# Kernel tuning notes

Hardware: AMD Instinct MI355X
Metric: run time of the kernel (lower is better)

## Reference

```python
import jax, jax.numpy as jnp
import numpy as np

N_QUBITS = 12
N_LAYERS = 6
N_CLASSES = 10
BATCH = 4096


def _rot_matrix(phi, theta, omega):
    # PennyLane Rot(phi, theta, omega) = RZ(omega) @ RY(theta) @ RZ(phi)
    ct = jnp.cos(theta / 2).astype(jnp.complex64)
    st = jnp.sin(theta / 2).astype(jnp.complex64)
    ep = jnp.exp(-0.5j * (phi + omega)).astype(jnp.complex64)  # e^{-i(phi+omega)/2}
    em = jnp.exp(-0.5j * (phi - omega)).astype(jnp.complex64)  # e^{-i(phi-omega)/2}
    row0 = jnp.stack([ep * ct, -jnp.conj(em) * st])
    row1 = jnp.stack([em * st, jnp.conj(ep) * ct])
    return jnp.stack([row0, row1])  # [2, 2] complex64


def _apply_1q(state, U, q):
    # state: [B] + [2]*n ; apply 2x2 gate U on qubit axis q
    s = jnp.moveaxis(state, q + 1, -1)
    s = jnp.einsum('...i,ji->...j', s, U)
    return jnp.moveaxis(s, -1, q + 1)


def _apply_cnot(state, c, t):
    # flip target axis where control bit == 1
    s = jnp.moveaxis(state, (c + 1, t + 1), (1, 2))
    s = jnp.concatenate([s[:, :1], jnp.flip(s[:, 1:2], axis=2)], axis=1)
    return jnp.moveaxis(s, (1, 2), (c + 1, t + 1))


def _pauliz_signs(n):
    idx = np.arange(2 ** n)
    bits = (idx[None, :] >> (n - 1 - np.arange(n))[:, None]) & 1  # [n, 2^n]
    return jnp.asarray(1.0 - 2.0 * bits, dtype=jnp.float32)


def _quantum_forward(x, q_params):
    B, n = x.shape
    # rotation encoding: RY(x_q)|0> = [cos(x/2), sin(x/2)] -> product state
    c = jnp.cos(x / 2)
    s = jnp.sin(x / 2)
    state = jnp.ones((B, 1), dtype=jnp.complex64)
    for q in range(n):
        amp = jnp.stack([c[:, q], s[:, q]], axis=-1).astype(jnp.complex64)  # [B, 2]
        state = (state[:, :, None] * amp[:, None, :]).reshape(B, -1)
    state = state.reshape((B,) + (2,) * n)
    # StronglyEntanglingLayers: per-layer Rot on every wire, then CNOT ring with range r
    for l in range(N_LAYERS):
        for q in range(n):
            U = _rot_matrix(q_params[l, q, 0], q_params[l, q, 1], q_params[l, q, 2])
            state = _apply_1q(state, U, q)
        r = (l % (n - 1)) + 1
        for q in range(n):
            state = _apply_cnot(state, q, (q + r) % n)
    probs = (jnp.abs(state) ** 2).reshape(B, -1).astype(jnp.float32)  # [B, 2^n]
    signs = _pauliz_signs(n)  # [n, 2^n]
    return probs @ signs.T  # PauliZ expvals, [B, n]


def setup_inputs() -> dict:
    key = jax.random.key(0)
    k1, k2, k3, k4 = jax.random.split(key, 4)
    x = jax.random.normal(k1, (BATCH, N_QUBITS), dtype=jnp.float32)
    q_params = 0.01 * jax.random.normal(k2, (N_LAYERS, N_QUBITS, 3), dtype=jnp.float32)
    lim = 1.0 / np.sqrt(N_QUBITS)
    fc_w = jax.random.uniform(k3, (N_CLASSES, N_QUBITS), jnp.float32, -lim, lim)
    fc_b = jax.random.uniform(k4, (N_CLASSES,), jnp.float32, -lim, lim)
    return {"x": x, "q_params": q_params, "fc_w": fc_w, "fc_b": fc_b}


def reference(x, q_params, fc_w, fc_b):
    expvals = _quantum_forward(x, q_params)  # [B, n_qubits]
    return expvals @ fc_w.T + fc_b  # logits [B, n_classes]
```

## Files before the change

kernel.cpp:

```cpp
#include <hip/hip_runtime.h>
#include <hip/hip_fp16.h>

#define NQ 12
#define NL 6
#define NC 10
#define DIM 4096
#define TPB 256
#define NPASS 18

typedef _Float16 half8_t __attribute__((ext_vector_type(8)));
typedef __fp16 fp16x2 __attribute__((ext_vector_type(2)));
typedef float f32x4 __attribute__((ext_vector_type(4)));
typedef unsigned u32;

struct PassT {
    u32 colL[4];
    u32 colW[2];
    u32 colT[2];
    u32 colS[4];
};
struct QCArgs {
    PassT P[NPASS];
    u32 GcolP0[8];
    u32 tLogP0[4];
    u32 sLogP0[4];
    u32 tidMask[NQ];
    u32 tab16[NQ];
};

__device__ __forceinline__ u32 pkrtz(float a, float b) {
    fp16x2 r = __builtin_amdgcn_cvt_pkrtz(a, b);
    return __builtin_bit_cast(u32, r);
}
__device__ __forceinline__ u32 packh2(float a, float b) {
    __half2 h;
    h.x = __float2half(a);
    h.y = __float2half(b);
    return __builtin_bit_cast(u32, h);
}
__device__ __forceinline__ float r16(float v) { return __half2float(__float2half(v)); }

__global__ __launch_bounds__(TPB) void prep_k(const float* __restrict__ qp, uint4* __restrict__ ws)
{
    __shared__ float4 gmat[NL * NQ];
    const unsigned tid = threadIdx.x;
    const unsigned lane = tid & 63;
    const unsigned wv = tid >> 6;
    const float SCALE = 1.00048828125f;

    if (tid < NL * NQ) {
        float phi = qp[tid * 3 + 0];
        float th  = qp[tid * 3 + 1];
        float om  = qp[tid * 3 + 2];
        float st_, ct, sa, ca, sb, cb;
        sincosf(0.5f * th, &st_, &ct);
        sincosf(0.5f * (phi + om), &sa, &ca);
        sincosf(0.5f * (phi - om), &sb, &cb);
        gmat[tid] = make_float4(ca * ct, -sa * ct, cb * st_, -sb * st_);
    }
    __syncthreads();

    const int i16 = lane & 15;
    const int sb0 = (int)(lane >> 4) * 4;
    for (int k = (int)wv; k < NPASS; k += 4) {
        const int gb = (k / 3) * NQ + (k % 3) * 4;
        u32 fH[4], fL[4];
        #pragma unroll
        for (int jj = 0; jj < 4; ++jj) {
            int s = sb0 + jj;
            float cre = 1.0f, cim = 0.0f;
            #pragma unroll
            for (int g = 0; g < 4; ++g) {
                float4 gq = gmat[gb + g];
                int ib = (i16 >> g) & 1, sb2 = (s >> g) & 1;
                float er, ei;
                if (ib == 0 && sb2 == 0)      { er =  gq.x; ei =  gq.y; }
                else if (ib == 0 && sb2 == 1) { er = -gq.z; ei =  gq.w; }
                else if (ib == 1 && sb2 == 0) { er =  gq.z; ei =  gq.w; }
                else                          { er =  gq.x; ei = -gq.y; }
                float nre = cre * er - cim * ei;
                float nim = cre * ei + cim * er;
                cre = nre; cim = nim;
            }
            float mi = -cim * SCALE;
            cre *= SCALE;
            fH[jj] = packh2(cre, mi);
            fL[jj] = packh2(cre - r16(cre), mi - r16(mi));
        }
        uint4 h = make_uint4(fH[0], fH[1], fH[2], fH[3]);
        uint4 l = make_uint4(fL[0], fL[1], fL[2], fL[3]);
        uint4 hI, lI;
        hI.x = ((h.x << 16) | (h.x >> 16)) ^ 0x8000u;
        hI.y = ((h.y << 16) | (h.y >> 16)) ^ 0x8000u;
        hI.z = ((h.z << 16) | (h.z >> 16)) ^ 0x8000u;
        hI.w = ((h.w << 16) | (h.w >> 16)) ^ 0x8000u;
        lI.x = ((l.x << 16) | (l.x >> 16)) ^ 0x8000u;
        lI.y = ((l.y << 16) | (l.y >> 16)) ^ 0x8000u;
        lI.z = ((l.z << 16) | (l.z >> 16)) ^ 0x8000u;
        lI.w = ((l.w << 16) | (l.w >> 16)) ^ 0x8000u;
        ws[0 * 1152 + k * 64 + lane] = h;
        ws[1 * 1152 + k * 64 + lane] = l;
        ws[2 * 1152 + k * 64 + lane] = hI;
        ws[3 * 1152 + k * 64 + lane] = lI;
    }
}

__global__ __launch_bounds__(TPB, 6) void qsim_k(
    const float* __restrict__ x,
    const float* __restrict__ fcw, const float* __restrict__ fcb,
    float* __restrict__ out, int B, const uint4* __restrict__ ws, QCArgs K)
{
    __shared__ u32 stamp[DIM];
    __shared__ float csn[NQ], snn[NQ];
    __shared__ float zred[4 * NQ];
    __shared__ float zfin[NQ];

    const unsigned tid = threadIdx.x;
    const unsigned lane = tid & 63;
    const unsigned wv = tid >> 6;
    const int blk = blockIdx.x;

    if (tid < NQ) {
        float s, c;
        sincosf(0.5f * x[(size_t)blk * NQ + tid], &s, &c);
        csn[tid] = c; snn[tid] = s;
    }
    __syncthreads();

    u32 mb[8];
    #pragma unroll
    for (int b = 0; b < 8; ++b) mb[b] = (u32)(-(int)((tid >> b) & 1u));

    float pr[16];

    {
        uint4 fh  = ws[0 * 1152 + lane];
        uint4 fl  = ws[1 * 1152 + lane];
        uint4 fhI = ws[2 * 1152 + lane];
        uint4 flI = ws[3 * 1152 + lane];
        half8_t AreH = __builtin_bit_cast(half8_t, fh);
        half8_t AreL = __builtin_bit_cast(half8_t, fl);
        half8_t AimH = __builtin_bit_cast(half8_t, fhI);
        half8_t AimL = __builtin_bit_cast(half8_t, flI);

        float csr[NQ], snr[NQ];
        #pragma unroll
        for (int p = 0; p < NQ; ++p) { csr[p] = csn[11 - p]; snr[p] = snn[11 - p]; }
        u32 Glog = 0;
        #pragma unroll
        for (int b = 0; b < 8; ++b) Glog ^= mb[b] & K.GcolP0[b];

        const PassT& P = K.P[0];
        u32 A = (mb[0] & P.colL[0]) ^ (mb[1] & P.colL[1]) ^ (mb[2] & P.colL[2]) ^ (mb[3] & P.colL[3])
              ^ (mb[4] & P.colS[2]) ^ (mb[5] & P.colS[3]) ^ (mb[6] & P.colW[0]) ^ (mb[7] & P.colW[1]);
        const u32 o1 = P.colS[0], o2 = P.colS[1], o3 = o1 ^ o2;
        const u32 t1 = P.colT[0], t2 = P.colT[1];
        const u32 tf[4] = {0u, t1, t2, t1 ^ t2};

        #pragma unroll
        for (int t = 0; t < 4; ++t) {
            u32 bb[4];
            #pragma unroll
            for (int jj = 0; jj < 4; ++jj) {
                u32 idx = Glog ^ K.tLogP0[t] ^ K.sLogP0[jj];
                float amp = 1.0f;
                #pragma unroll
                for (int p = 0; p < NQ; ++p)
                    amp *= ((idx >> p) & 1) ? snr[p] : csr[p];
                bb[jj] = pkrtz(amp, 0.0f);
            }
            half8_t Bf = __builtin_bit_cast(half8_t, make_uint4(bb[0], bb[1], bb[2], bb[3]));
            f32x4 zc = {0.0f, 0.0f, 0.0f, 0.0f};
            f32x4 Dre = __builtin_amdgcn_mfma_f32_16x16x32_f16(
                AreH, Bf, __builtin_amdgcn_mfma_f32_16x16x32_f16(AreL, Bf, zc, 0, 0, 0), 0, 0, 0);
            f32x4 Dim = __builtin_amdgcn_mfma_f32_16x16x32_f16(
                AimH, Bf, __builtin_amdgcn_mfma_f32_16x16x32_f16(AimL, Bf, zc, 0, 0, 0), 0, 0, 0);
            u32 At = A ^ tf[t];
            *(u32*)((char*)stamp + At)        = pkrtz(Dre[0], Dim[0]);
            *(u32*)((char*)stamp + (At ^ o1)) = pkrtz(Dre[1], Dim[1]);
            *(u32*)((char*)stamp + (At ^ o2)) = pkrtz(Dre[2], Dim[2]);
            *(u32*)((char*)stamp + (At ^ o3)) = pkrtz(Dre[3], Dim[3]);
        }
    }

    #pragma unroll
    for (int k = 1; k < NPASS; ++k) {
        uint4 fh  = ws[0 * 1152 + k * 64 + lane];
        uint4 fl  = ws[1 * 1152 + k * 64 + lane];
        uint4 fhI = ws[2 * 1152 + k * 64 + lane];
        uint4 flI = ws[3 * 1152 + k * 64 + lane];
        half8_t AreH = __builtin_bit_cast(half8_t, fh);
        half8_t AreL = __builtin_bit_cast(half8_t, fl);
        half8_t AimH = __builtin_bit_cast(half8_t, fhI);
        half8_t AimL = __builtin_bit_cast(half8_t, flI);

        __syncthreads();
        const PassT& P = K.P[k];
        u32 A = (mb[0] & P.colL[0]) ^ (mb[1] & P.colL[1]) ^ (mb[2] & P.colL[2]) ^ (mb[3] & P.colL[3])
              ^ (mb[4] & P.colS[2]) ^ (mb[5] & P.colS[3]) ^ (mb[6] & P.colW[0]) ^ (mb[7] & P.colW[1]);
        const u32 o1 = P.colS[0], o2 = P.colS[1], o3 = o1 ^ o2;
        const u32 t1 = P.colT[0], t2 = P.colT[1];
        const u32 tf[4] = {0u, t1, t2, t1 ^ t2};

        #pragma unroll
        for (int t = 0; t < 4; ++t) {
            u32 At = A ^ tf[t];
            u32 b0 = *(const u32*)((const char*)stamp + At);
            u32 b1 = *(const u32*)((const char*)stamp + (At ^ o1));
            u32 b2 = *(const u32*)((const char*)stamp + (At ^ o2));
            u32 b3 = *(const u32*)((const char*)stamp + (At ^ o3));
            half8_t Bf = __builtin_bit_cast(half8_t, make_uint4(b0, b1, b2, b3));
            f32x4 zc = {0.0f, 0.0f, 0.0f, 0.0f};
            f32x4 Dre = __builtin_amdgcn_mfma_f32_16x16x32_f16(
                AreH, Bf, __builtin_amdgcn_mfma_f32_16x16x32_f16(AreL, Bf, zc, 0, 0, 0), 0, 0, 0);
            f32x4 Dim = __builtin_amdgcn_mfma_f32_16x16x32_f16(
                AimH, Bf, __builtin_amdgcn_mfma_f32_16x16x32_f16(AimL, Bf, zc, 0, 0, 0), 0, 0, 0);
            if (k < NPASS - 1) {
                *(u32*)((char*)stamp + At)        = pkrtz(Dre[0], Dim[0]);
                *(u32*)((char*)stamp + (At ^ o1)) = pkrtz(Dre[1], Dim[1]);
                *(u32*)((char*)stamp + (At ^ o2)) = pkrtz(Dre[2], Dim[2]);
                *(u32*)((char*)stamp + (At ^ o3)) = pkrtz(Dre[3], Dim[3]);
            } else {
                pr[t * 4 + 0] = fmaf(Dre[0], Dre[0], Dim[0] * Dim[0]);
                pr[t * 4 + 1] = fmaf(Dre[1], Dre[1], Dim[1] * Dim[1]);
                pr[t * 4 + 2] = fmaf(Dre[2], Dre[2], Dim[2] * Dim[2]);
                pr[t * 4 + 3] = fmaf(Dre[3], Dre[3], Dim[3] * Dim[3]);
            }
        }
    }

    float z[NQ];
    #pragma unroll
    for (int q = 0; q < NQ; ++q) {
        float base = (__popc(K.tidMask[q] & tid) & 1) ? -1.0f : 1.0f;
        u32 tb = K.tab16[q];
        float acc = 0.0f;
        #pragma unroll
        for (int idx = 0; idx < 16; ++idx) {
            float sgn = ((tb >> idx) & 1u) ? -base : base;
            acc = fmaf(sgn, pr[idx], acc);
        }
        z[q] = acc;
    }
    #pragma unroll
    for (int q = 0; q < NQ; ++q) {
        float v = z[q];
        #pragma unroll
        for (int o = 1; o < 64; o <<= 1) v += __shfl_xor(v, o, 64);
        z[q] = v;
    }
    if ((tid & 63) == 0) {
        #pragma unroll
        for (int q = 0; q < NQ; ++q) zred[wv * NQ + q] = z[q];
    }
    __syncthreads();
    if (tid < NQ)
        zfin[tid] = zred[tid] + zred[NQ + tid] + zred[2 * NQ + tid] + zred[3 * NQ + tid];
    __syncthreads();

    if (tid < NC) {
        float acc = fcb[tid];
        #pragma unroll
        for (int q = 0; q < NQ; ++q) acc = fmaf(fcw[tid * NQ + q], zfin[q], acc);
        out[(size_t)blk * NC + tid] = acc;
    }
}

static void inv12(const unsigned Ain[12], unsigned Ai[12]) {
    unsigned M[12], I[12];
    for (int i = 0; i < 12; ++i) { M[i] = Ain[i]; I[i] = 1u << i; }
    for (int c = 0; c < 12; ++c) {
        int pr = -1;
        for (int r2 = c; r2 < 12; ++r2) if ((M[r2] >> c) & 1u) { pr = r2; break; }
        unsigned tm = M[c]; M[c] = M[pr]; M[pr] = tm;
        tm = I[c]; I[c] = I[pr]; I[pr] = tm;
        for (int r2 = 0; r2 < 12; ++r2)
            if (r2 != c && ((M[r2] >> c) & 1u)) { M[r2] ^= M[c]; I[r2] ^= I[c]; }
    }
    for (int i = 0; i < 12; ++i) Ai[i] = I[i];
}
static unsigned lcg(unsigned& s) { s = s * 1664525u + 1013904223u; return s >> 8; }
static int pc(unsigned v) { return __builtin_popcount(v); }

extern "C" void kernel_launch(void* const* d_in, const int* in_sizes, int n_in,
                              void* d_out, int out_size, void* d_ws, size_t ws_size,
                              hipStream_t stream) {
    const float* x    = (const float*)d_in[0];
    const float* qp   = (const float*)d_in[1];
    const float* fc_w = (const float*)d_in[2];
    const float* fc_b = (const float*)d_in[3];
    float* out = (float*)d_out;
    int B = in_sizes[0] / NQ;

    unsigned L[12];
    for (int i = 0; i < 12; ++i) L[i] = 1u << i;
    static unsigned vAll[NPASS][4], rAll[NPASS][4], vcAll[NPASS][16];
    static int posAll[NPASS][8];
    for (int l = 0; l < NL; ++l) {
        unsigned Linv[12];
        inv12(L, Linv);
        for (int m = 0; m < 3; ++m) {
            int k = l * 3 + m;
            for (int j = 0; j < 4; ++j) {
                int qq = 4 * m + j, bb = 11 - qq;
                rAll[k][j] = L[bb];
                unsigned vv = 0;
                for (int i = 0; i < 12; ++i) vv |= ((Linv[i] >> bb) & 1u) << i;
                vAll[k][j] = vv;
            }
            unsigned w[4]; int piv[4];
            for (int j = 0; j < 4; ++j) {
                w[j] = vAll[k][j];
                for (int k2 = 0; k2 < j; ++k2)
                    if ((w[j] >> piv[k2]) & 1u) w[j] ^= w[k2];
                piv[j] = __builtin_ctz(w[j]);
            }
            bool ispiv[12] = {};
            for (int j = 0; j < 4; ++j) ispiv[piv[j]] = true;
            int c = 0;
            for (int pos = 0; pos < 12; ++pos)
                if (!ispiv[pos]) posAll[k][c++] = pos;
            for (int s = 0; s < 16; ++s) {
                unsigned vc = 0;
                for (int j = 0; j < 4; ++j) if ((s >> j) & 1) vc ^= vAll[k][j];
                vcAll[k][s] = vc;
            }
        }
        int rr = l + 1;
        for (int q = 0; q < 12; ++q) {
            int tq = (q + rr) % 12;
            L[11 - tq] ^= L[11 - q];
        }
    }
    unsigned rfin[12];
    for (int q = 0; q < 12; ++q) rfin[q] = L[11 - q];

    unsigned labels[12];
    unsigned seed = 0x5EED321u;
    auto lab5 = [&](unsigned v) -> unsigned {
        unsigned r = 0;
        for (int pos = 0; pos < 12; ++pos) if ((v >> pos) & 1u) r ^= labels[pos];
        return r & 31u;
    };
    bool okAll = false;
    for (int att = 0; att < 300000 && !okAll; ++att) {
        for (int i = 0; i < 12; ++i) labels[i] = 1u + (lcg(seed) % 31u);
        okAll = true;
        for (int k = 0; k < NPASS && okAll; ++k) {
            unsigned Labj[4];
            for (int j = 0; j < 4; ++j) Labj[j] = lab5(vAll[k][j]);
            unsigned ech[5], low[5]; int rk = 0;
            unsigned v2l = Labj[2];
            if (v2l) { ech[rk] = v2l; low[rk] = v2l & (0u - v2l); ++rk; }
            int got = 0;
            for (int b = 0; b < 8 && got < 4; ++b) {
                int p = posAll[k][b];
                unsigned f = labels[p] & 31u;
                for (int j = 0; j < 4; ++j) if ((rAll[k][j] >> p) & 1u) f ^= Labj[j];
                unsigned vv = f & 31u;
                for (int i = 0; i < rk; ++i) if (vv & low[i]) vv ^= ech[i];
                if (vv) { ech[rk] = vv; low[rk] = vv & (0u - vv); ++rk; ++got; }
            }
            okAll = (rk == 5);
        }
    }
    for (int k = 0; k < NPASS; ++k) {
        unsigned Labj[4];
        for (int j = 0; j < 4; ++j) Labj[j] = lab5(vAll[k][j]);
        unsigned ech[5], low[5]; int rk = 0;
        unsigned v2l = Labj[2];
        if (v2l) { ech[rk] = v2l; low[rk] = v2l & (0u - v2l); ++rk; }
        int used[8] = {}, chosen[4], nch = 0;
        for (int b = 0; b < 8 && nch < 4; ++b) {
            int p = posAll[k][b];
            unsigned f = labels[p] & 31u;
            for (int j = 0; j < 4; ++j) if ((rAll[k][j] >> p) & 1u) f ^= Labj[j];
            unsigned vv = f & 31u;
            for (int i = 0; i < rk; ++i) if (vv & low[i]) vv ^= ech[i];
            if (vv) { ech[rk] = vv; low[rk] = vv & (0u - vv); ++rk; chosen[nch++] = b; used[b] = 1; }
        }
        for (int b = 0; b < 8 && nch < 4; ++b)
            if (!used[b]) { chosen[nch++] = b; used[b] = 1; }
        int outp[8]; int c2 = 0;
        for (int j = 0; j < nch; ++j) outp[c2++] = posAll[k][chosen[j]];
        for (int b = 0; b < 8; ++b) if (!used[b]) outp[c2++] = posAll[k][b];
        for (int b = 0; b < 8; ++b) posAll[k][b] = outp[b];
    }

    unsigned Trow[12];
    {
        unsigned ech[12], low[12]; int rk = 0;
        auto addrow = [&](unsigned vr) -> bool {
            unsigned vv = vr;
            for (int i = 0; i < rk; ++i) if (vv & low[i]) vv ^= ech[i];
            if (!vv) return false;
            ech[rk] = vv; low[rk] = vv & (0u - vv); ++rk;
            return true;
        };
        int idx = 0;
        for (int i = 0; i < 5; ++i) {
            unsigned r = 0;
            for (int pos = 0; pos < 12; ++pos) r |= ((labels[pos] >> i) & 1u) << pos;
            if (addrow(r)) Trow[idx++] = r;
        }
        int tries = 0;
        while (idx < 12 && tries < 100000) {
            unsigned rr2 = lcg(seed) & 4095u;
            if (rr2 && addrow(rr2)) Trow[idx++] = rr2;
            ++tries;
        }
        for (int i = 0; i < 12 && idx < 12; ++i)
            if (addrow(1u << i)) Trow[idx++] = 1u << i;
    }
    unsigned Tcol[12];
    for (int pos = 0; pos < 12; ++pos) {
        unsigned o = 0;
        for (int i = 0; i < 12; ++i) o |= ((Trow[i] >> pos) & 1u) << i;
        Tcol[pos] = o;
    }
    auto Tmap = [&](unsigned m) -> unsigned {
        unsigned o = 0;
        for (int i = 0; i < 12; ++i) o |= (unsigned)(pc(Trow[i] & m) & 1) << i;
        return o;
    };

    QCArgs K;
    __builtin_memset(&K, 0, sizeof(K));
    for (int k = 0; k < NPASS; ++k) {
        unsigned Dt[4];
        for (int j = 0; j < 4; ++j) Dt[j] = Tmap(vAll[k][j]);
        auto foldcol = [&](int p) -> unsigned {
            unsigned col = Tcol[p];
            for (int j = 0; j < 4; ++j)
                if ((rAll[k][j] >> p) & 1u) col ^= Dt[j];
            return col << 2;
        };
        for (int b = 0; b < 4; ++b) K.P[k].colL[b] = foldcol(posAll[k][b]);
        K.P[k].colW[0] = foldcol(posAll[k][4]);
        K.P[k].colW[1] = foldcol(posAll[k][5]);
        K.P[k].colT[0] = foldcol(posAll[k][6]);
        K.P[k].colT[1] = foldcol(posAll[k][7]);
        for (int j = 0; j < 4; ++j) K.P[k].colS[j] = Dt[j] << 2;
    }
    for (int b = 0; b < 4; ++b) K.GcolP0[b] = 1u << posAll[0][b];
    K.GcolP0[4] = vAll[0][2];
    K.GcolP0[5] = vAll[0][3];
    K.GcolP0[6] = 1u << posAll[0][4];
    K.GcolP0[7] = 1u << posAll[0][5];
    for (int t = 0; t < 4; ++t)
        K.tLogP0[t] = ((t & 1) ? (1u << posAll[0][6]) : 0u) ^ ((t & 2) ? (1u << posAll[0][7]) : 0u);
    for (int jj = 0; jj < 4; ++jj)
        K.sLogP0[jj] = ((jj & 1) ? vAll[0][0] : 0u) ^ ((jj & 2) ? vAll[0][1] : 0u);

    const int kl = NPASS - 1;
    for (int q = 0; q < NQ; ++q) {
        auto wsbit = [&](int p) -> unsigned {
            unsigned bit = (rfin[q] >> p) & 1u;
            for (int j = 0; j < 4; ++j)
                bit ^= ((rAll[kl][j] >> p) & 1u) & (unsigned)(pc(rfin[q] & vAll[kl][j]) & 1);
            return bit;
        };
        unsigned tm = 0;
        for (int b = 0; b < 4; ++b) tm |= wsbit(posAll[kl][b]) << b;
        tm |= (unsigned)(pc(rfin[q] & vAll[kl][2]) & 1) << 4;
        tm |= (unsigned)(pc(rfin[q] & vAll[kl][3]) & 1) << 5;
        tm |= wsbit(posAll[kl][4]) << 6;
        tm |= wsbit(posAll[kl][5]) << 7;
        K.tidMask[q] = tm;
        unsigned tb0 = wsbit(posAll[kl][6]), tb1 = wsbit(posAll[kl][7]);
        unsigned j0 = (unsigned)(pc(rfin[q] & vAll[kl][0]) & 1);
        unsigned j1 = (unsigned)(pc(rfin[q] & vAll[kl][1]) & 1);
        unsigned tab = 0;
        for (int t = 0; t < 4; ++t)
            for (int jj = 0; jj < 4; ++jj) {
                unsigned s2 = ((t & 1) ? tb0 : 0u) ^ ((t & 2) ? tb1 : 0u)
                            ^ ((jj & 1) ? j0 : 0u) ^ ((jj & 2) ? j1 : 0u);
                tab |= s2 << (t * 4 + jj);
            }
        K.tab16[q] = tab;
    }

    uint4* wsv = (uint4*)d_ws;
    prep_k<<<1, TPB, 0, stream>>>(qp, wsv);
    qsim_k<<<B, TPB, 0, stream>>>(x, fc_w, fc_b, out, B, wsv, K);
}
```

Measured before the change: 102.8 us.

## Process two batch samples per block with interleaved uint2 LDS state

Each block now simulates two batch samples at once. The state is stored as uint2 pairs in shared memory, and the fp16 gate fragments loaded from the workspace are reused for both samples' MFMAs. The host-side bank-swizzle label search is changed from 5-bit to 4-bit labels, with the address shift moved from <<2 to <<3 to match the 8-byte elements. This halves the grid and the per-sample gate loads and barriers, and gives each wave more independent MFMA work. In exchange it doubles LDS use (32KB per block) and register pressure, and lowers the occupancy hint from 6 to 4.

```diff
diff --git a/kernel.cpp b/kernel.cpp
--- a/kernel.cpp
+++ b/kernel.cpp
@@ -105,25 +105,31 @@
     }
 }
 
-__global__ __launch_bounds__(TPB, 6) void qsim_k(
+__global__ __launch_bounds__(TPB, 4) void qsim_k(
     const float* __restrict__ x,
     const float* __restrict__ fcw, const float* __restrict__ fcb,
     float* __restrict__ out, int B, const uint4* __restrict__ ws, QCArgs K)
 {
-    __shared__ u32 stamp[DIM];
-    __shared__ float csn[NQ], snn[NQ];
-    __shared__ float zred[4 * NQ];
-    __shared__ float zfin[NQ];
+    __shared__ uint2 stamp[DIM];
+    __shared__ float2 csn[NQ], snn[NQ];
+    __shared__ float2 zred[4 * NQ];
+    __shared__ float2 zfin[NQ];
 
     const unsigned tid = threadIdx.x;
     const unsigned lane = tid & 63;
     const unsigned wv = tid >> 6;
     const int blk = blockIdx.x;
-
-    if (tid < NQ) {
+    const int b0 = blk * 2, b1 = blk * 2 + 1;
+
+    if (tid < 2 * NQ) {
+        int half = tid / NQ;
+        int q = tid - half * NQ;
+        int bb = blk * 2 + half;
+        float xx = (bb < B) ? x[(size_t)bb * NQ + q] : 0.0f;
         float s, c;
-        sincosf(0.5f * x[(size_t)blk * NQ + tid], &s, &c);
-        csn[tid] = c; snn[tid] = s;
+        sincosf(0.5f * xx, &s, &c);
+        if (half == 0) { csn[q].x = c; snn[q].x = s; }
+        else           { csn[q].y = c; snn[q].y = s; }
     }
     __syncthreads();
 
@@ -131,7 +137,7 @@
     #pragma unroll
     for (int b = 0; b < 8; ++b) mb[b] = (u32)(-(int)((tid >> b) & 1u));
 
-    float pr[16];
+    float pr0[16], pr1[16];
 
     {
         uint4 fh  = ws[0 * 1152 + lane];
@@ -143,7 +149,7 @@
         half8_t AimH = __builtin_bit_cast(half8_t, fhI);
         half8_t AimL = __builtin_bit_cast(half8_t, flI);
 
-        float csr[NQ], snr[NQ];
+        float2 csr[NQ], snr[NQ];
         #pragma unroll
         for (int p = 0; p < NQ; ++p) { csr[p] = csn[11 - p]; snr[p] = snn[11 - p]; }
         u32 Glog = 0;
@@ -159,27 +165,35 @@
 
         #pragma unroll
         for (int t = 0; t < 4; ++t) {
-            u32 bb[4];
+            u32 bb0[4], bb1[4];
             #pragma unroll
             for (int jj = 0; jj < 4; ++jj) {
                 u32 idx = Glog ^ K.tLogP0[t] ^ K.sLogP0[jj];
-                float amp = 1.0f;
+                float a0 = 1.0f, a1 = 1.0f;
                 #pragma unroll
-                for (int p = 0; p < NQ; ++p)
-                    amp *= ((idx >> p) & 1) ? snr[p] : csr[p];
-                bb[jj] = pkrtz(amp, 0.0f);
-            }
-            half8_t Bf = __builtin_bit_cast(half8_t, make_uint4(bb[0], bb[1], bb[2], bb[3]));
+                for (int p = 0; p < NQ; ++p) {
+                    float2 v = ((idx >> p) & 1) ? snr[p] : csr[p];
+                    a0 *= v.x; a1 *= v.y;
+                }
+                bb0[jj] = pkrtz(a0, 0.0f);
+                bb1[jj] = pkrtz(a1, 0.0f);
+            }
+            half8_t Bf0 = __builtin_bit_cast(half8_t, make_uint4(bb0[0], bb0[1], bb0[2], bb0[3]));
+            half8_t Bf1 = __builtin_bit_cast(half8_t, make_uint4(bb1[0], bb1[1], bb1[2], bb1[3]));
             f32x4 zc = {0.0f, 0.0f, 0.0f, 0.0f};
-            f32x4 Dre = __builtin_amdgcn_mfma_f32_16x16x32_f16(
-                AreH, Bf, __builtin_amdgcn_mfma_f32_16x16x32_f16(AreL, Bf, zc, 0, 0, 0), 0, 0, 0);
-            f32x4 Dim = __builtin_amdgcn_mfma_f32_16x16x32_f16(
-                AimH, Bf, __builtin_amdgcn_mfma_f32_16x16x32_f16(AimL, Bf, zc, 0, 0, 0), 0, 0, 0);
+            f32x4 Dre0 = __builtin_amdgcn_mfma_f32_16x16x32_f16(
+                AreH, Bf0, __builtin_amdgcn_mfma_f32_16x16x32_f16(AreL, Bf0, zc, 0, 0, 0), 0, 0, 0);
+            f32x4 Dim0 = __builtin_amdgcn_mfma_f32_16x16x32_f16(
+                AimH, Bf0, __builtin_amdgcn_mfma_f32_16x16x32_f16(AimL, Bf0, zc, 0, 0, 0), 0, 0, 0);
+            f32x4 Dre1 = __builtin_amdgcn_mfma_f32_16x16x32_f16(
+                AreH, Bf1, __builtin_amdgcn_mfma_f32_16x16x32_f16(AreL, Bf1, zc, 0, 0, 0), 0, 0, 0);
+            f32x4 Dim1 = __builtin_amdgcn_mfma_f32_16x16x32_f16(
+                AimH, Bf1, __builtin_amdgcn_mfma_f32_16x16x32_f16(AimL, Bf1, zc, 0, 0, 0), 0, 0, 0);
             u32 At = A ^ tf[t];
-            *(u32*)((char*)stamp + At)        = pkrtz(Dre[0], Dim[0]);
-            *(u32*)((char*)stamp + (At ^ o1)) = pkrtz(Dre[1], Dim[1]);
-            *(u32*)((char*)stamp + (At ^ o2)) = pkrtz(Dre[2], Dim[2]);
-            *(u32*)((char*)stamp + (At ^ o3)) = pkrtz(Dre[3], Dim[3]);
+            *(uint2*)((char*)stamp + At)        = make_uint2(pkrtz(Dre0[0], Dim0[0]), pkrtz(Dre1[0], Dim1[0]));
+            *(uint2*)((char*)stamp + (At ^ o1)) = make_uint2(pkrtz(Dre0[1], Dim0[1]), pkrtz(Dre1[1], Dim1[1]));
+            *(uint2*)((char*)stamp + (At ^ o2)) = make_uint2(pkrtz(Dre0[2], Dim0[2]), pkrtz(Dre1[2], Dim1[2]));
+            *(uint2*)((char*)stamp + (At ^ o3)) = make_uint2(pkrtz(Dre0[3], Dim0[3]), pkrtz(Dre1[3], Dim1[3]));
         }
     }
 
@@ -205,64 +219,81 @@
         #pragma unroll
         for (int t = 0; t < 4; ++t) {
             u32 At = A ^ tf[t];
-            u32 b0 = *(const u32*)((const char*)stamp + At);
-            u32 b1 = *(const u32*)((const char*)stamp + (At ^ o1));
-            u32 b2 = *(const u32*)((const char*)stamp + (At ^ o2));
-            u32 b3 = *(const u32*)((const char*)stamp + (At ^ o3));
-            half8_t Bf = __builtin_bit_cast(half8_t, make_uint4(b0, b1, b2, b3));
+            uint2 r0 = *(const uint2*)((const char*)stamp + At);
+            uint2 r1 = *(const uint2*)((const char*)stamp + (At ^ o1));
+            uint2 r2 = *(const uint2*)((const char*)stamp + (At ^ o2));
+            uint2 r3 = *(const uint2*)((const char*)stamp + (At ^ o3));
+            half8_t Bf0 = __builtin_bit_cast(half8_t, make_uint4(r0.x, r1.x, r2.x, r3.x));
+            half8_t Bf1 = __builtin_bit_cast(half8_t, make_uint4(r0.y, r1.y, r2.y, r3.y));
             f32x4 zc = {0.0f, 0.0f, 0.0f, 0.0f};
-            f32x4 Dre = __builtin_amdgcn_mfma_f32_16x16x32_f16(
-                AreH, Bf, __builtin_amdgcn_mfma_f32_16x16x32_f16(AreL, Bf, zc, 0, 0, 0), 0, 0, 0);
-            f32x4 Dim = __builtin_amdgcn_mfma_f32_16x16x32_f16(
-                AimH, Bf, __builtin_amdgcn_mfma_f32_16x16x32_f16(AimL, Bf, zc, 0, 0, 0), 0, 0, 0);
+            f32x4 Dre0 = __builtin_amdgcn_mfma_f32_16x16x32_f16(
+                AreH, Bf0, __builtin_amdgcn_mfma_f32_16x16x32_f16(AreL, Bf0, zc, 0, 0, 0), 0, 0, 0);
+            f32x4 Dim0 = __builtin_amdgcn_mfma_f32_16x16x32_f16(
+                AimH, Bf0, __builtin_amdgcn_mfma_f32_16x16x32_f16(AimL, Bf0, zc, 0, 0, 0), 0, 0, 0);
+            f32x4 Dre1 = __builtin_amdgcn_mfma_f32_16x16x32_f16(
+                AreH, Bf1, __builtin_amdgcn_mfma_f32_16x16x32_f16(AreL, Bf1, zc, 0, 0, 0), 0, 0, 0);
+            f32x4 Dim1 = __builtin_amdgcn_mfma_f32_16x16x32_f16(
+                AimH, Bf1, __builtin_amdgcn_mfma_f32_16x16x32_f16(AimL, Bf1, zc, 0, 0, 0), 0, 0, 0);
             if (k < NPASS - 1) {
-                *(u32*)((char*)stamp + At)        = pkrtz(Dre[0], Dim[0]);
-                *(u32*)((char*)stamp + (At ^ o1)) = pkrtz(Dre[1], Dim[1]);
-                *(u32*)((char*)stamp + (At ^ o2)) = pkrtz(Dre[2], Dim[2]);
-                *(u32*)((char*)stamp + (At ^ o3)) = pkrtz(Dre[3], Dim[3]);
+                *(uint2*)((char*)stamp + At)        = make_uint2(pkrtz(Dre0[0], Dim0[0]), pkrtz(Dre1[0], Dim1[0]));
+                *(uint2*)((char*)stamp + (At ^ o1)) = make_uint2(pkrtz(Dre0[1], Dim0[1]), pkrtz(Dre1[1], Dim1[1]));
+                *(uint2*)((char*)stamp + (At ^ o2)) = make_uint2(pkrtz(Dre0[2], Dim0[2]), pkrtz(Dre1[2], Dim1[2]));
+                *(uint2*)((char*)stamp + (At ^ o3)) = make_uint2(pkrtz(Dre0[3], Dim0[3]), pkrtz(Dre1[3], Dim1[3]));
             } else {
-                pr[t * 4 + 0] = fmaf(Dre[0], Dre[0], Dim[0] * Dim[0]);
-                pr[t * 4 + 1] = fmaf(Dre[1], Dre[1], Dim[1] * Dim[1]);
-                pr[t * 4 + 2] = fmaf(Dre[2], Dre[2], Dim[2] * Dim[2]);
-                pr[t * 4 + 3] = fmaf(Dre[3], Dre[3], Dim[3] * Dim[3]);
-            }
-        }
-    }
-
-    float z[NQ];
+                #pragma unroll
+                for (int i = 0; i < 4; ++i) {
+                    pr0[t * 4 + i] = fmaf(Dre0[i], Dre0[i], Dim0[i] * Dim0[i]);
+                    pr1[t * 4 + i] = fmaf(Dre1[i], Dre1[i], Dim1[i] * Dim1[i]);
+                }
+            }
+        }
+    }
+
+    float2 z[NQ];
     #pragma unroll
     for (int q = 0; q < NQ; ++q) {
         float base = (__popc(K.tidMask[q] & tid) & 1) ? -1.0f : 1.0f;
         u32 tb = K.tab16[q];
-        float acc = 0.0f;
+        float a0 = 0.0f, a1 = 0.0f;
         #pragma unroll
         for (int idx = 0; idx < 16; ++idx) {
             float sgn = ((tb >> idx) & 1u) ? -base : base;
-            acc = fmaf(sgn, pr[idx], acc);
-        }
-        z[q] = acc;
+            a0 = fmaf(sgn, pr0[idx], a0);
+            a1 = fmaf(sgn, pr1[idx], a1);
+        }
+        z[q].x = a0; z[q].y = a1;
     }
     #pragma unroll
     for (int q = 0; q < NQ; ++q) {
-        float v = z[q];
-        #pragma unroll
-        for (int o = 1; o < 64; o <<= 1) v += __shfl_xor(v, o, 64);
-        z[q] = v;
+        float vx = z[q].x, vy = z[q].y;
+        #pragma unroll
+        for (int o = 1; o < 64; o <<= 1) {
+            vx += __shfl_xor(vx, o, 64);
+            vy += __shfl_xor(vy, o, 64);
+        }
+        z[q].x = vx; z[q].y = vy;
     }
     if ((tid & 63) == 0) {
         #pragma unroll
         for (int q = 0; q < NQ; ++q) zred[wv * NQ + q] = z[q];
     }
     __syncthreads();
-    if (tid < NQ)
-        zfin[tid] = zred[tid] + zred[NQ + tid] + zred[2 * NQ + tid] + zred[3 * NQ + tid];
+    if (tid < NQ) {
+        float2 a = zred[tid], b2 = zred[NQ + tid], c = zred[2 * NQ + tid], d = zred[3 * NQ + tid];
+        zfin[tid] = make_float2(a.x + b2.x + c.x + d.x, a.y + b2.y + c.y + d.y);
+    }
     __syncthreads();
 
     if (tid < NC) {
-        float acc = fcb[tid];
-        #pragma unroll
-        for (int q = 0; q < NQ; ++q) acc = fmaf(fcw[tid * NQ + q], zfin[q], acc);
-        out[(size_t)blk * NC + tid] = acc;
+        float acc0 = fcb[tid], acc1 = fcb[tid];
+        #pragma unroll
+        for (int q = 0; q < NQ; ++q) {
+            float w = fcw[tid * NQ + q];
+            acc0 = fmaf(w, zfin[q].x, acc0);
+            acc1 = fmaf(w, zfin[q].y, acc1);
+        }
+        out[(size_t)b0 * NC + tid] = acc0;
+        if (b1 < B) out[(size_t)b1 * NC + tid] = acc1;
     }
 }
 
@@ -336,46 +367,41 @@
     for (int q = 0; q < 12; ++q) rfin[q] = L[11 - q];
 
     unsigned labels[12];
-    unsigned seed = 0x5EED321u;
-    auto lab5 = [&](unsigned v) -> unsigned {
+    unsigned seed = 0xA11CE21u;
+    auto lab4 = [&](unsigned v) -> unsigned {
         unsigned r = 0;
         for (int pos = 0; pos < 12; ++pos) if ((v >> pos) & 1u) r ^= labels[pos];
-        return r & 31u;
+        return r & 15u;
     };
     bool okAll = false;
-    for (int att = 0; att < 300000 && !okAll; ++att) {
-        for (int i = 0; i < 12; ++i) labels[i] = 1u + (lcg(seed) % 31u);
+    for (int att = 0; att < 400000 && !okAll; ++att) {
+        for (int i = 0; i < 12; ++i) labels[i] = 1u + (lcg(seed) % 15u);
         okAll = true;
         for (int k = 0; k < NPASS && okAll; ++k) {
             unsigned Labj[4];
-            for (int j = 0; j < 4; ++j) Labj[j] = lab5(vAll[k][j]);
-            unsigned ech[5], low[5]; int rk = 0;
-            unsigned v2l = Labj[2];
-            if (v2l) { ech[rk] = v2l; low[rk] = v2l & (0u - v2l); ++rk; }
-            int got = 0;
-            for (int b = 0; b < 8 && got < 4; ++b) {
+            for (int j = 0; j < 4; ++j) Labj[j] = lab4(vAll[k][j]);
+            unsigned ech[4], low[4]; int rk = 0;
+            for (int b = 0; b < 8 && rk < 4; ++b) {
                 int p = posAll[k][b];
-                unsigned f = labels[p] & 31u;
+                unsigned f = labels[p] & 15u;
                 for (int j = 0; j < 4; ++j) if ((rAll[k][j] >> p) & 1u) f ^= Labj[j];
-                unsigned vv = f & 31u;
+                unsigned vv = f & 15u;
                 for (int i = 0; i < rk; ++i) if (vv & low[i]) vv ^= ech[i];
-                if (vv) { ech[rk] = vv; low[rk] = vv & (0u - vv); ++rk; ++got; }
-            }
-            okAll = (rk == 5);
+                if (vv) { ech[rk] = vv; low[rk] = vv & (0u - vv); ++rk; }
+            }
+            okAll = (rk == 4);
         }
     }
     for (int k = 0; k < NPASS; ++k) {
         unsigned Labj[4];
-        for (int j = 0; j < 4; ++j) Labj[j] = lab5(vAll[k][j]);
-        unsigned ech[5], low[5]; int rk = 0;
-        unsigned v2l = Labj[2];
-        if (v2l) { ech[rk] = v2l; low[rk] = v2l & (0u - v2l); ++rk; }
+        for (int j = 0; j < 4; ++j) Labj[j] = lab4(vAll[k][j]);
+        unsigned ech[4], low[4]; int rk = 0;
         int used[8] = {}, chosen[4], nch = 0;
         for (int b = 0; b < 8 && nch < 4; ++b) {
             int p = posAll[k][b];
-            unsigned f = labels[p] & 31u;
+            unsigned f = labels[p] & 15u;
             for (int j = 0; j < 4; ++j) if ((rAll[k][j] >> p) & 1u) f ^= Labj[j];
-            unsigned vv = f & 31u;
+            unsigned vv = f & 15u;
             for (int i = 0; i < rk; ++i) if (vv & low[i]) vv ^= ech[i];
             if (vv) { ech[rk] = vv; low[rk] = vv & (0u - vv); ++rk; chosen[nch++] = b; used[b] = 1; }
         }
@@ -398,7 +424,7 @@
             return true;
         };
         int idx = 0;
-        for (int i = 0; i < 5; ++i) {
+        for (int i = 0; i < 4; ++i) {
             unsigned r = 0;
             for (int pos = 0; pos < 12; ++pos) r |= ((labels[pos] >> i) & 1u) << pos;
             if (addrow(r)) Trow[idx++] = r;
@@ -433,14 +459,14 @@
             unsigned col = Tcol[p];
             for (int j = 0; j < 4; ++j)
                 if ((rAll[k][j] >> p) & 1u) col ^= Dt[j];
-            return col << 2;
+            return col << 3;
         };
         for (int b = 0; b < 4; ++b) K.P[k].colL[b] = foldcol(posAll[k][b]);
         K.P[k].colW[0] = foldcol(posAll[k][4]);
         K.P[k].colW[1] = foldcol(posAll[k][5]);
         K.P[k].colT[0] = foldcol(posAll[k][6]);
         K.P[k].colT[1] = foldcol(posAll[k][7]);
-        for (int j = 0; j < 4; ++j) K.P[k].colS[j] = Dt[j] << 2;
+        for (int j = 0; j < 4; ++j) K.P[k].colS[j] = Dt[j] << 3;
     }
     for (int b = 0; b < 4; ++b) K.GcolP0[b] = 1u << posAll[0][b];
     K.GcolP0[4] = vAll[0][2];
@@ -482,5 +508,6 @@
 
     uint4* wsv = (uint4*)d_ws;
     prep_k<<<1, TPB, 0, stream>>>(qp, wsv);
-    qsim_k<<<B, TPB, 0, stream>>>(x, fc_w, fc_b, out, B, wsv, K);
+    int nblk = (B + 1) / 2;
+    qsim_k<<<nblk, TPB, 0, stream>>>(x, fc_w, fc_b, out, B, wsv, K);
 }
```

New measurement: 103.9 us. About the same (+1.1%).
